# Performance work log

Measured on AMD Instinct MI355X. Metric: run time of the kernel, lower is better.

## Reference

```python
import jax, jax.numpy as jnp
import numpy as np
import math

B, S_IMG, S_TXT = 1, 2048, 256
D_MODEL, HEADS, HEAD_DIM = 3072, 24, 128
INNER = HEADS * HEAD_DIM
EPS = 1e-6


def _rmsnorm(x, scale):
    # flax-style RMSNorm over last dim, fp32 stats
    x32 = x.astype(jnp.float32)
    var = jnp.mean(x32 * x32, axis=-1, keepdims=True)
    return ((x32 * jax.lax.rsqrt(var + EPS)).astype(x.dtype)) * scale


def _rope(x, cos, sin):
    # x: [B,S,H,D]; cos,sin: [S,D]; interleaved-pair rotation (use_real_unbind_dim=-1)
    c = cos[None, :, None, :].astype(jnp.float32)
    s = sin[None, :, None, :].astype(jnp.float32)
    xp = x.reshape(*x.shape[:-1], -1, 2)
    x_rot = jnp.stack([-xp[..., 1], xp[..., 0]], axis=-1).reshape(x.shape)
    return (x.astype(jnp.float32) * c + x_rot.astype(jnp.float32) * s).astype(x.dtype)


def setup_inputs() -> dict:
    key = jax.random.key(0)
    ks = jax.random.split(key, 16)
    w = lambda k, shp: jax.random.normal(k, shp, jnp.float32) * 0.02
    S = S_TXT + S_IMG
    pos = jnp.arange(S, dtype=jnp.float32)
    inv_freq = 1.0 / (10000.0 ** (jnp.arange(0, HEAD_DIM, 2, dtype=jnp.float32) / HEAD_DIM))
    ang = pos[:, None] * inv_freq[None, :]  # [S, D/2]
    cos = jnp.repeat(jnp.cos(ang), 2, axis=-1)  # [S, D] paired layout
    sin = jnp.repeat(jnp.sin(ang), 2, axis=-1)
    return {
        'hidden_states': jax.random.normal(ks[0], (B, S_IMG, D_MODEL), jnp.float32),
        'encoder_hidden_states': jax.random.normal(ks[1], (B, S_TXT, D_MODEL), jnp.float32),
        'cos': cos,
        'sin': sin,
        'wq': w(ks[2], (D_MODEL, INNER)),
        'wk': w(ks[3], (D_MODEL, INNER)),
        'wv': w(ks[4], (D_MODEL, INNER)),
        'wq_add': w(ks[5], (D_MODEL, INNER)),
        'wk_add': w(ks[6], (D_MODEL, INNER)),
        'wv_add': w(ks[7], (D_MODEL, INNER)),
        'bq_add': w(ks[8], (INNER,)),
        'bk_add': w(ks[9], (INNER,)),
        'bv_add': w(ks[10], (INNER,)),
        'norm_q': jnp.ones((HEAD_DIM,), jnp.float32),
        'norm_k': jnp.ones((HEAD_DIM,), jnp.float32),
        'norm_add_q': jnp.ones((HEAD_DIM,), jnp.float32),
        'norm_add_k': jnp.ones((HEAD_DIM,), jnp.float32),
        'w_out': w(ks[11], (INNER, D_MODEL)),
        'b_out': w(ks[12], (D_MODEL,)),
        'w_add_out': w(ks[13], (INNER, D_MODEL)),
        'b_add_out': w(ks[14], (D_MODEL,)),
    }


def reference(hidden_states, encoder_hidden_states, cos, sin, wq, wk, wv,
              wq_add, wk_add, wv_add, bq_add, bk_add, bv_add,
              norm_q, norm_k, norm_add_q, norm_add_k,
              w_out, b_out, w_add_out, b_add_out):
    St = encoder_hidden_states.shape[1]
    heads = lambda x: x.reshape(x.shape[0], x.shape[1], HEADS, HEAD_DIM)
    # image-token q/k/v + QK RMSNorm
    q = _rmsnorm(heads(hidden_states @ wq), norm_q)
    k = _rmsnorm(heads(hidden_states @ wk), norm_k)
    v = heads(hidden_states @ wv)
    # encoder-token q/k/v (biased projections) + QK RMSNorm
    eq = _rmsnorm(heads(encoder_hidden_states @ wq_add + bq_add), norm_add_q)
    ek = _rmsnorm(heads(encoder_hidden_states @ wk_add + bk_add), norm_add_k)
    ev = heads(encoder_hidden_states @ wv_add + bv_add)
    # encoder tokens concatenated first
    q = jnp.concatenate([eq, q], axis=1)
    k = jnp.concatenate([ek, k], axis=1)
    v = jnp.concatenate([ev, v], axis=1)
    q = _rope(q, cos, sin)
    k = _rope(k, cos, sin)
    # naive softmax attention
    scale = 1.0 / math.sqrt(HEAD_DIM)
    attn = jnp.einsum('bshd,bthd->bhst', q, k) * scale
    attn = jax.nn.softmax(attn, axis=-1)
    out = jnp.einsum('bhst,bthd->bshd', attn, v)
    out = out.reshape(out.shape[0], out.shape[1], -1)
    # split back into encoder / image streams and apply output projections
    enc_out = out[:, :St] @ w_add_out + b_add_out
    img_out = out[:, St:] @ w_out + b_out
    return (img_out, enc_out)
```

## Files before the change

### kernel.cpp

```cpp
#include <hip/hip_runtime.h>
#include <hip/hip_bf16.h>

typedef unsigned short u16;
typedef unsigned int   u32;
typedef __bf16 bf16x8 __attribute__((ext_vector_type(8)));
typedef float  f32x4  __attribute__((ext_vector_type(4)));

#define SEQ   2304
#define DM    3072
#define NH    24
#define HD    128
#define S_TXT 256
#define S_IMG 2048
#define SCALE 0.08838834764831845f

__device__ __forceinline__ u16 f2bf(float x) {
  u32 u = __float_as_uint(x);
  u += 0x7fffu + ((u >> 16) & 1u);
  return (u16)(u >> 16);
}
__device__ __forceinline__ float bf2f(u16 b) {
  return __uint_as_float(((u32)b) << 16);
}
__device__ __forceinline__ f32x4 zero4() { f32x4 z = {0.f, 0.f, 0.f, 0.f}; return z; }
__device__ __forceinline__ u32 cvtpk(float lo, float hi) {
  u32 r;
  asm("v_cvt_pk_bf16_f32 %0, %1, %2" : "=v"(r) : "v"(lo), "v"(hi));
  return r;
}

#define GLDS16(gp, lp) __builtin_amdgcn_global_load_lds( \
    (__attribute__((address_space(1))) void*)(gp),       \
    (__attribute__((address_space(3))) void*)(lp), 16, 0, 0)

__global__ __launch_bounds__(256) void conv_bf16_k(const float* __restrict__ src,
                                                   u16* __restrict__ dst, int n4) {
  int i = blockIdx.x * 256 + threadIdx.x;
  if (i >= n4) return;
  float4 v = ((const float4*)src)[i];
  ushort4 o;
  o.x = f2bf(v.x); o.y = f2bf(v.y); o.z = f2bf(v.z); o.w = f2bf(v.w);
  ((ushort4*)dst)[i] = o;
}

struct WP { const float* s[8]; u16* d[8]; };

__global__ __launch_bounds__(256) void w_transpose_k(WP p) {
  __shared__ float tile[32][33];
  const float* __restrict__ src = p.s[blockIdx.z];
  u16* __restrict__ dst = p.d[blockIdx.z];
  const int c0 = blockIdx.x * 32, r0 = blockIdx.y * 32;
  const int tx = threadIdx.x & 31, ty = threadIdx.x >> 5;
#pragma unroll
  for (int i = 0; i < 4; ++i)
    tile[ty + i*8][tx] = src[(size_t)(r0 + ty + i*8) * DM + c0 + tx];
  __syncthreads();
#pragma unroll
  for (int i = 0; i < 4; ++i)
    dst[(size_t)(c0 + ty + i*8) * DM + r0 + tx] = f2bf(tile[tx][ty + i*8]);
}

__global__ __launch_bounds__(256) void v_transpose_k(const u16* __restrict__ V,
                                                     u16* __restrict__ Vt) {
  __shared__ u16 tile[32][34];
  const int h = blockIdx.z;
  const int t0 = blockIdx.x * 32, d0 = blockIdx.y * 32;
  const int tx = threadIdx.x & 31, ty = threadIdx.x >> 5;
#pragma unroll
  for (int i = 0; i < 4; ++i)
    tile[ty + i*8][tx] = V[((size_t)h * SEQ + t0 + ty + i*8) * HD + d0 + tx];
  __syncthreads();
#pragma unroll
  for (int i = 0; i < 4; ++i)
    Vt[((size_t)h * HD + d0 + ty + i*8) * SEQ + t0 + tx] = tile[tx][ty + i*8];
}

struct GArgs {
  const u16* A;
  const u16* Bimg0; const u16* Bimg1; const u16* Bimg2;
  const u16* Benc0; const u16* Benc1; const u16* Benc2;
  const float* bEnc0; const float* bEnc1; const float* bEnc2;
  const float* bImg;
  void* out0; void* out1; void* out2;
  int mode;
};

__global__ __launch_bounds__(256) void gemm_bt_k(GArgs p) {
  __shared__ __attribute__((aligned(128))) char As[128*128];
  __shared__ __attribute__((aligned(128))) char Bs[128*128];
  const int bz = blockIdx.z;
  const int bm = blockIdx.x, bn = blockIdx.y;
  const bool enc = (bm < 2);
  const u16* __restrict__ Bm = (bz == 0) ? (enc ? p.Benc0 : p.Bimg0)
                             : (bz == 1) ? (enc ? p.Benc1 : p.Bimg1)
                                         : (enc ? p.Benc2 : p.Bimg2);
  const float* __restrict__ bias = enc ? ((bz == 0) ? p.bEnc0 : (bz == 1) ? p.bEnc1 : p.bEnc2)
                                       : p.bImg;
  void* out = (bz == 0) ? p.out0 : (bz == 1) ? p.out1 : p.out2;
  const int tid = threadIdx.x;
  const int w = tid >> 6, l = tid & 63;
  const int wr = w >> 1, wc = w & 1;

  f32x4 acc[4][4];
#pragma unroll
  for (int mi = 0; mi < 4; ++mi)
#pragma unroll
    for (int ni = 0; ni < 4; ++ni) acc[mi][ni] = zero4();

  const int srow  = l >> 3;
  const int scolb = ((l & 7) ^ srow) << 4;
  const char* Ag = (const char*)(p.A + (size_t)(bm*128 + w*32) * DM) + (size_t)srow * (DM*2) + scolb;
  const char* Bg = (const char*)(Bm  + (size_t)(bn*128 + w*32) * DM) + (size_t)srow * (DM*2) + scolb;
  char* AsW = As + (w*32) * 128;
  char* BsW = Bs + (w*32) * 128;

  for (int kt = 0; kt < DM/64; ++kt) {
#pragma unroll
    for (int i = 0; i < 4; ++i) {
      GLDS16(Ag + (size_t)i*8*(DM*2) + kt*128, AsW + i*8*128);
      GLDS16(Bg + (size_t)i*8*(DM*2) + kt*128, BsW + i*8*128);
    }
    __syncthreads();
#pragma unroll
    for (int kk = 0; kk < 2; ++kk) {
      bf16x8 af[4], bfr[4];
#pragma unroll
      for (int mi = 0; mi < 4; ++mi) {
        const int row = wr*64 + mi*16 + (l & 15);
        const int cb  = ((kk << 6) + ((l >> 4) << 4)) ^ ((row & 7) << 4);
        af[mi] = *(const bf16x8*)(As + row*128 + cb);
      }
#pragma unroll
      for (int ni = 0; ni < 4; ++ni) {
        const int row = wc*64 + ni*16 + (l & 15);
        const int cb  = ((kk << 6) + ((l >> 4) << 4)) ^ ((row & 7) << 4);
        bfr[ni] = *(const bf16x8*)(Bs + row*128 + cb);
      }
#pragma unroll
      for (int mi = 0; mi < 4; ++mi)
#pragma unroll
        for (int ni = 0; ni < 4; ++ni)
          acc[mi][ni] = __builtin_amdgcn_mfma_f32_16x16x32_bf16(af[mi], bfr[ni], acc[mi][ni], 0, 0, 0);
    }
    __syncthreads();
  }

#pragma unroll
  for (int mi = 0; mi < 4; ++mi) {
    const int mbase = bm*128 + wr*64 + mi*16 + ((l >> 4) << 2);
#pragma unroll
    for (int ni = 0; ni < 4; ++ni) {
      const int ncol = bn*128 + wc*64 + ni*16 + (l & 15);
      const float bv = bias ? bias[ncol] : 0.f;
#pragma unroll
      for (int r = 0; r < 4; ++r) {
        const float v = acc[mi][ni][r] + bv;
        const int row = mbase + r;
        if (p.mode == 0) {
          ((u16*)out)[((size_t)bn * SEQ + row) * HD + (ncol & 127)] = f2bf(v);
        } else {
          const size_t orow = (row < S_TXT) ? (size_t)(S_IMG + row) : (size_t)(row - S_TXT);
          ((float*)out)[orow * DM + ncol] = v;
        }
      }
    }
  }
}

__global__ __launch_bounds__(256) void qk_norm_rope_k(
    const u16* __restrict__ Qf, const u16* __restrict__ Kf,
    u16* __restrict__ Qb, u16* __restrict__ Kb,
    const float* __restrict__ cosT, const float* __restrict__ sinT,
    const float* __restrict__ nq, const float* __restrict__ nk,
    const float* __restrict__ naq, const float* __restrict__ nak) {
  const int gw = (blockIdx.x * 256 + threadIdx.x) >> 6;
  const int l = threadIdx.x & 63;
  const int which = (gw >= NH * SEQ) ? 1 : 0;
  const int rem = which ? (gw - NH * SEQ) : gw;
  const int h = rem / SEQ, t = rem % SEQ;
  const size_t base = ((size_t)h * SEQ + t) * HD + l * 2;
  const ushort2 xb = *(const ushort2*)((which ? Kf : Qf) + base);
  const float x0 = bf2f(xb.x), x1 = bf2f(xb.y);
  float ss = x0*x0 + x1*x1;
#pragma unroll
  for (int msk = 1; msk < 64; msk <<= 1) ss += __shfl_xor(ss, msk, 64);
  const float rr = rsqrtf(ss * (1.0f/128.0f) + 1e-6f);
  const float* nw = which ? (t < S_TXT ? nak : nk) : (t < S_TXT ? naq : nq);
  const float n0 = x0 * rr * nw[l*2], n1 = x1 * rr * nw[l*2 + 1];
  const float c = cosT[(size_t)t * HD + l*2], sn = sinT[(size_t)t * HD + l*2];
  float o0 = n0 * c - n1 * sn;
  float o1 = n1 * c + n0 * sn;
  if (!which) { o0 *= SCALE; o1 *= SCALE; }
  ushort2 ob; ob.x = f2bf(o0); ob.y = f2bf(o1);
  *(ushort2*)((which ? Kb : Qb) + base) = ob;
}

__global__ __launch_bounds__(256) void attn_k(
    const u16* __restrict__ Q, const u16* __restrict__ K,
    const u16* __restrict__ Vt, u16* __restrict__ O) {
  __shared__ __attribute__((aligned(128))) char Kl[2][64*256];
  __shared__ __attribute__((aligned(128))) char Vl[2][128*128];
  __shared__ __attribute__((aligned(128))) char Pl[4][2048];
  const int orig = blockIdx.x;
  const int lin = (orig & 7) * 54 + (orig >> 3);
  const int h = lin / 18, qb = lin % 18;
  const int tid = threadIdx.x, w = tid >> 6, l = tid & 63;
  const int g = l >> 4, q16 = l & 15;
  const int NT = SEQ / 64;

  const u16* Qh = Q  + ((size_t)h * SEQ + qb*128 + w*32) * HD;
  const u16* Kh = K  + (size_t)h * SEQ * HD;
  const u16* Vh = Vt + (size_t)h * HD * SEQ;

  bf16x8 qf[2][4];
#pragma unroll
  for (int qt = 0; qt < 2; ++qt)
#pragma unroll
    for (int kf = 0; kf < 4; ++kf)
      qf[qt][kf] = *(const bf16x8*)(Qh + (qt*16 + q16) * HD + kf*32 + g*8);

  f32x4 o[2][8];
#pragma unroll
  for (int qt = 0; qt < 2; ++qt)
#pragma unroll
    for (int db = 0; db < 8; ++db) o[qt][db] = zero4();
  float m[2]  = {-3e38f, -3e38f};
  float rl[2] = {0.f, 0.f};

  const int vswz = ((l & 7) ^ (l >> 3)) << 4;
  const int pswz = (q16 & 7) << 4;

  auto STAGE = [&](int buf, int kb) {
#pragma unroll
    for (int i = 0; i < 4; ++i) {
      const int rloc = i*4 + (l >> 4);
      const int colb = ((l & 15) << 4) ^ ((rloc & 7) << 4);
      GLDS16((const char*)Kh + ((size_t)(kb*64 + w*16 + rloc)) * 256 + colb,
             &Kl[buf][(w*16 + i*4) * 256]);
    }
#pragma unroll
    for (int i = 0; i < 4; ++i) {
      const int rloc = w*32 + i*8 + (l >> 3);
      GLDS16((const char*)Vh + (size_t)rloc * (SEQ*2) + kb*128 + vswz,
             &Vl[buf][(w*32 + i*8) * 128]);
    }
  };

  STAGE(0, 0);
  int cur = 0;

  for (int kb = 0; kb < NT; ++kb) {
    if (kb + 1 < NT) {
      STAGE(cur ^ 1, kb + 1);
      asm volatile("s_waitcnt vmcnt(8)" ::: "memory");
    } else {
      asm volatile("s_waitcnt vmcnt(0)" ::: "memory");
    }
    __builtin_amdgcn_s_barrier();
    __builtin_amdgcn_sched_barrier(0);

    const char* Kb_ = Kl[cur];
    const char* Vb_ = Vl[cur];

    f32x4 s[2][4];
#pragma unroll
    for (int qt = 0; qt < 2; ++qt)
#pragma unroll
      for (int mi = 0; mi < 4; ++mi) s[qt][mi] = zero4();
    __builtin_amdgcn_s_setprio(1);
#pragma unroll
    for (int mi = 0; mi < 4; ++mi) {
      const int row = mi*16 + q16;
      bf16x8 kfr[4];
#pragma unroll
      for (int kf = 0; kf < 4; ++kf) {
        const int cb = ((kf << 6) + (g << 4)) ^ ((row & 7) << 4);
        kfr[kf] = *(const bf16x8*)(Kb_ + row*256 + cb);
      }
#pragma unroll
      for (int kf = 0; kf < 4; ++kf) {
        s[0][mi] = __builtin_amdgcn_mfma_f32_16x16x32_bf16(kfr[kf], qf[0][kf], s[0][mi], 0, 0, 0);
        s[1][mi] = __builtin_amdgcn_mfma_f32_16x16x32_bf16(kfr[kf], qf[1][kf], s[1][mi], 0, 0, 0);
      }
    }
    __builtin_amdgcn_s_setprio(0);

    float rsv[2];
    bf16x8 pa[2][2];
    char* Pw = Pl[w];
#pragma unroll
    for (int qt = 0; qt < 2; ++qt) {
      float mx = s[qt][0][0];
#pragma unroll
      for (int mi = 0; mi < 4; ++mi)
#pragma unroll
        for (int r = 0; r < 4; ++r) mx = fmaxf(mx, s[qt][mi][r]);
      mx = fmaxf(mx, __shfl_xor(mx, 16, 64));
      mx = fmaxf(mx, __shfl_xor(mx, 32, 64));
      const float mn = fmaxf(m[qt], mx);
      rsv[qt] = __expf(m[qt] - mn);
      m[qt] = mn;
      float sum = 0.f;
#pragma unroll
      for (int mi = 0; mi < 4; ++mi) {
        f32x4 t = s[qt][mi];
#pragma unroll
        for (int r = 0; r < 4; ++r) { t[r] = __expf(t[r] - mn); sum += t[r]; }
        s[qt][mi] = t;
      }
      sum += __shfl_xor(sum, 16, 64);
      sum += __shfl_xor(sum, 32, 64);
      rl[qt] = rl[qt] * rsv[qt] + sum;
#pragma unroll
      for (int mi = 0; mi < 4; ++mi) {
        uint2 pk;
        pk.x = cvtpk(s[qt][mi][0], s[qt][mi][1]);
        pk.y = cvtpk(s[qt][mi][2], s[qt][mi][3]);
        *(uint2*)(Pw + ((q16*128 + mi*32 + g*8) ^ pswz)) = pk;
      }
#pragma unroll
      for (int kblk = 0; kblk < 2; ++kblk)
        pa[qt][kblk] = *(const bf16x8*)(Pw + ((q16*128 + kblk*64 + g*16) ^ pswz));
    }

#pragma unroll
    for (int qt = 0; qt < 2; ++qt) {
      float rs4[4];
#pragma unroll
      for (int r = 0; r < 4; ++r)
        rs4[r] = __shfl(rsv[qt], (g << 4) + (g << 2) + r, 64);
#pragma unroll
      for (int db = 0; db < 8; ++db) {
        f32x4 t = o[qt][db];
#pragma unroll
        for (int r = 0; r < 4; ++r) t[r] *= rs4[r];
        o[qt][db] = t;
      }
    }

    __builtin_amdgcn_s_setprio(1);
#pragma unroll
    for (int kblk = 0; kblk < 2; ++kblk)
#pragma unroll
      for (int db = 0; db < 8; ++db) {
        const int vrow = db*16 + q16;
        const int vcb  = ((kblk << 6) + (g << 4)) ^ ((vrow & 7) << 4);
        bf16x8 vb = *(const bf16x8*)(Vb_ + vrow*128 + vcb);
        o[0][db] = __builtin_amdgcn_mfma_f32_16x16x32_bf16(pa[0][kblk], vb, o[0][db], 0, 0, 0);
        o[1][db] = __builtin_amdgcn_mfma_f32_16x16x32_bf16(pa[1][kblk], vb, o[1][db], 0, 0, 0);
      }
    __builtin_amdgcn_s_setprio(0);

    asm volatile("s_waitcnt lgkmcnt(0)" ::: "memory");
    __builtin_amdgcn_s_barrier();
    __builtin_amdgcn_sched_barrier(0);
    cur ^= 1;
  }

#pragma unroll
  for (int qt = 0; qt < 2; ++qt) {
    float inv4[4];
#pragma unroll
    for (int r = 0; r < 4; ++r)
      inv4[r] = 1.f / __shfl(rl[qt], (g << 4) + (g << 2) + r, 64);
#pragma unroll
    for (int db = 0; db < 8; ++db)
#pragma unroll
      for (int r = 0; r < 4; ++r) {
        const int token = qb*128 + w*32 + qt*16 + g*4 + r;
        const int col = h*HD + db*16 + q16;
        O[(size_t)token * DM + col] = f2bf(o[qt][db][r] * inv4[r]);
      }
  }
}

extern "C" void kernel_launch(void* const* d_in, const int* in_sizes, int n_in,
                              void* d_out, int out_size, void* d_ws, size_t ws_size,
                              hipStream_t stream) {
  const float* hidden = (const float*)d_in[0];
  const float* ench   = (const float*)d_in[1];
  const float* cosT   = (const float*)d_in[2];
  const float* sinT   = (const float*)d_in[3];
  const float* wq  = (const float*)d_in[4];
  const float* wk  = (const float*)d_in[5];
  const float* wv  = (const float*)d_in[6];
  const float* wqa = (const float*)d_in[7];
  const float* wka = (const float*)d_in[8];
  const float* wva = (const float*)d_in[9];
  const float* bqa = (const float*)d_in[10];
  const float* bka = (const float*)d_in[11];
  const float* bva = (const float*)d_in[12];
  const float* nq  = (const float*)d_in[13];
  const float* nk  = (const float*)d_in[14];
  const float* naq = (const float*)d_in[15];
  const float* nak = (const float*)d_in[16];
  const float* w_out     = (const float*)d_in[17];
  const float* b_out     = (const float*)d_in[18];
  const float* w_add_out = (const float*)d_in[19];
  const float* b_add_out = (const float*)d_in[20];
  float* outp = (float*)d_out;
  (void)in_sizes; (void)n_in; (void)out_size; (void)ws_size;

  char* ws = (char*)d_ws;
  size_t off = 0;
  auto alloc = [&](size_t n) { char* p = ws + off; off += (n + 255) & ~(size_t)255; return p; };
  u16* wt[8];
  for (int i = 0; i < 8; ++i) wt[i] = (u16*)alloc((size_t)DM * DM * 2);
  u16* xb = (u16*)alloc((size_t)SEQ * DM * 2);
  u16* Qf = (u16*)alloc((size_t)NH * SEQ * HD * 2);
  u16* Kf = (u16*)alloc((size_t)NH * SEQ * HD * 2);
  u16* Vf = (u16*)alloc((size_t)NH * SEQ * HD * 2);
  u16* Qb = (u16*)alloc((size_t)NH * SEQ * HD * 2);
  u16* Kb = (u16*)alloc((size_t)NH * SEQ * HD * 2);
  u16* Vt = (u16*)alloc((size_t)NH * HD * SEQ * 2);
  u16* Ob = (u16*)alloc((size_t)SEQ * DM * 2);

  conv_bf16_k<<<(S_TXT*DM/4)/256, 256, 0, stream>>>(ench, xb, S_TXT*DM/4);
  conv_bf16_k<<<(S_IMG*DM/4)/256, 256, 0, stream>>>(hidden, xb + (size_t)S_TXT*DM, S_IMG*DM/4);

  WP wp;
  wp.s[0] = wq;  wp.s[1] = wk;  wp.s[2] = wv;
  wp.s[3] = wqa; wp.s[4] = wka; wp.s[5] = wva;
  wp.s[6] = w_out; wp.s[7] = w_add_out;
  for (int i = 0; i < 8; ++i) wp.d[i] = wt[i];
  w_transpose_k<<<dim3(96, 96, 8), 256, 0, stream>>>(wp);

  GArgs qkv;
  qkv.A = xb;
  qkv.Bimg0 = wt[0]; qkv.Bimg1 = wt[1]; qkv.Bimg2 = wt[2];
  qkv.Benc0 = wt[3]; qkv.Benc1 = wt[4]; qkv.Benc2 = wt[5];
  qkv.bEnc0 = bqa;   qkv.bEnc1 = bka;   qkv.bEnc2 = bva;
  qkv.bImg  = nullptr;
  qkv.out0 = Qf; qkv.out1 = Kf; qkv.out2 = Vf;
  qkv.mode = 0;
  gemm_bt_k<<<dim3(18, 24, 3), 256, 0, stream>>>(qkv);

  qk_norm_rope_k<<<(2*NH*SEQ)/4, 256, 0, stream>>>(Qf, Kf, Qb, Kb, cosT, sinT, nq, nk, naq, nak);
  v_transpose_k<<<dim3(SEQ/32, HD/32, NH), 256, 0, stream>>>(Vf, Vt);

  attn_k<<<432, 256, 0, stream>>>(Qb, Kb, Vt, Ob);

  GArgs op;
  op.A = Ob;
  op.Bimg0 = wt[6]; op.Bimg1 = wt[6]; op.Bimg2 = wt[6];
  op.Benc0 = wt[7]; op.Benc1 = wt[7]; op.Benc2 = wt[7];
  op.bEnc0 = b_add_out; op.bEnc1 = b_add_out; op.bEnc2 = b_add_out;
  op.bImg  = b_out;
  op.out0 = outp; op.out1 = outp; op.out2 = outp;
  op.mode = 1;
  gemm_bt_k<<<dim3(18, 24, 1), 256, 0, stream>>>(op);
}
```

Before: 781.0 us.

## Fuse QK RMSNorm, RoPE and V transpose into QKV GEMM epilogue

Folds the per-head RMSNorm, rotary embedding and Q scaling into the QKV projection GEMM epilogue, reducing row sums across the two column waves through shared memory. The V output is written already transposed, which removes the separate norm/rope and V-transpose kernels and their intermediate buffers. It also swizzles the GEMM block order into 8 groups over a 1D grid and widens the weight transpose to 64x64 tiles with float4 loads. The epilogue gets heavier and writes Vt with strided ushort4 stores that may coalesce poorly.

```diff
diff --git a/kernel.cpp b/kernel.cpp
--- a/kernel.cpp
+++ b/kernel.cpp
@@ -46,33 +46,32 @@
 struct WP { const float* s[8]; u16* d[8]; };
 
 __global__ __launch_bounds__(256) void w_transpose_k(WP p) {
-  __shared__ float tile[32][33];
+  __shared__ float tile[64][65];
   const float* __restrict__ src = p.s[blockIdx.z];
   u16* __restrict__ dst = p.d[blockIdx.z];
-  const int c0 = blockIdx.x * 32, r0 = blockIdx.y * 32;
-  const int tx = threadIdx.x & 31, ty = threadIdx.x >> 5;
-#pragma unroll
-  for (int i = 0; i < 4; ++i)
-    tile[ty + i*8][tx] = src[(size_t)(r0 + ty + i*8) * DM + c0 + tx];
+  const int c0 = blockIdx.x * 64, r0 = blockIdx.y * 64;
+  const int tr = threadIdx.x >> 4;
+  const int tc = threadIdx.x & 15;
+#pragma unroll
+  for (int i = 0; i < 4; ++i) {
+    float4 v = *(const float4*)&src[(size_t)(r0 + i*16 + tr) * DM + c0 + tc*4];
+    tile[i*16 + tr][tc*4 + 0] = v.x;
+    tile[i*16 + tr][tc*4 + 1] = v.y;
+    tile[i*16 + tr][tc*4 + 2] = v.z;
+    tile[i*16 + tr][tc*4 + 3] = v.w;
+  }
   __syncthreads();
 #pragma unroll
-  for (int i = 0; i < 4; ++i)
-    dst[(size_t)(c0 + ty + i*8) * DM + r0 + tx] = f2bf(tile[tx][ty + i*8]);
-}
-
-__global__ __launch_bounds__(256) void v_transpose_k(const u16* __restrict__ V,
-                                                     u16* __restrict__ Vt) {
-  __shared__ u16 tile[32][34];
-  const int h = blockIdx.z;
-  const int t0 = blockIdx.x * 32, d0 = blockIdx.y * 32;
-  const int tx = threadIdx.x & 31, ty = threadIdx.x >> 5;
-#pragma unroll
-  for (int i = 0; i < 4; ++i)
-    tile[ty + i*8][tx] = V[((size_t)h * SEQ + t0 + ty + i*8) * HD + d0 + tx];
-  __syncthreads();
-#pragma unroll
-  for (int i = 0; i < 4; ++i)
-    Vt[((size_t)h * HD + d0 + ty + i*8) * SEQ + t0 + tx] = tile[tx][ty + i*8];
+  for (int j = 0; j < 4; ++j) {
+    const int nloc = j*16 + tr;
+    const int kloc = tc*4;
+    ushort4 o;
+    o.x = f2bf(tile[kloc + 0][nloc]);
+    o.y = f2bf(tile[kloc + 1][nloc]);
+    o.z = f2bf(tile[kloc + 2][nloc]);
+    o.w = f2bf(tile[kloc + 3][nloc]);
+    *(ushort4*)&dst[(size_t)(c0 + nloc) * DM + r0 + kloc] = o;
+  }
 }
 
 struct GArgs {
@@ -81,6 +80,8 @@
   const u16* Benc0; const u16* Benc1; const u16* Benc2;
   const float* bEnc0; const float* bEnc1; const float* bEnc2;
   const float* bImg;
+  const float* cosT; const float* sinT;
+  const float* nq; const float* nk; const float* naq; const float* nak;
   void* out0; void* out1; void* out2;
   int mode;
 };
@@ -88,8 +89,12 @@
 __global__ __launch_bounds__(256) void gemm_bt_k(GArgs p) {
   __shared__ __attribute__((aligned(128))) char As[128*128];
   __shared__ __attribute__((aligned(128))) char Bs[128*128];
-  const int bz = blockIdx.z;
-  const int bm = blockIdx.x, bn = blockIdx.y;
+  const int chunk = gridDim.x >> 3;
+  const int wg = (blockIdx.x & 7) * chunk + (blockIdx.x >> 3);
+  const int bm = wg % 18;
+  const int bt = wg / 18;
+  const int bn = bt % 24;
+  const int bz = bt / 24;
   const bool enc = (bm < 2);
   const u16* __restrict__ Bm = (bz == 0) ? (enc ? p.Benc0 : p.Bimg0)
                              : (bz == 1) ? (enc ? p.Benc1 : p.Bimg1)
@@ -100,6 +105,7 @@
   const int tid = threadIdx.x;
   const int w = tid >> 6, l = tid & 63;
   const int wr = w >> 1, wc = w & 1;
+  const int g = l >> 4, q16 = l & 15;
 
   f32x4 acc[4][4];
 #pragma unroll
@@ -126,14 +132,14 @@
       bf16x8 af[4], bfr[4];
 #pragma unroll
       for (int mi = 0; mi < 4; ++mi) {
-        const int row = wr*64 + mi*16 + (l & 15);
-        const int cb  = ((kk << 6) + ((l >> 4) << 4)) ^ ((row & 7) << 4);
+        const int row = wr*64 + mi*16 + q16;
+        const int cb  = ((kk << 6) + (g << 4)) ^ ((row & 7) << 4);
         af[mi] = *(const bf16x8*)(As + row*128 + cb);
       }
 #pragma unroll
       for (int ni = 0; ni < 4; ++ni) {
-        const int row = wc*64 + ni*16 + (l & 15);
-        const int cb  = ((kk << 6) + ((l >> 4) << 4)) ^ ((row & 7) << 4);
+        const int row = wc*64 + ni*16 + q16;
+        const int cb  = ((kk << 6) + (g << 4)) ^ ((row & 7) << 4);
         bfr[ni] = *(const bf16x8*)(Bs + row*128 + cb);
       }
 #pragma unroll
@@ -145,54 +151,95 @@
     __syncthreads();
   }
 
-#pragma unroll
-  for (int mi = 0; mi < 4; ++mi) {
-    const int mbase = bm*128 + wr*64 + mi*16 + ((l >> 4) << 2);
-#pragma unroll
-    for (int ni = 0; ni < 4; ++ni) {
-      const int ncol = bn*128 + wc*64 + ni*16 + (l & 15);
-      const float bv = bias ? bias[ncol] : 0.f;
-#pragma unroll
-      for (int r = 0; r < 4; ++r) {
-        const float v = acc[mi][ni][r] + bv;
-        const int row = mbase + r;
-        if (p.mode == 0) {
-          ((u16*)out)[((size_t)bn * SEQ + row) * HD + (ncol & 127)] = f2bf(v);
-        } else {
+  if (p.mode == 0) {
+    if (bias) {
+#pragma unroll
+      for (int ni = 0; ni < 4; ++ni) {
+        const float bv = bias[bn*128 + wc*64 + ni*16 + q16];
+#pragma unroll
+        for (int mi = 0; mi < 4; ++mi) {
+          f32x4 t = acc[mi][ni];
+#pragma unroll
+          for (int r = 0; r < 4; ++r) t[r] += bv;
+          acc[mi][ni] = t;
+        }
+      }
+    }
+    if (bz == 2) {
+      u16* Vt_ = (u16*)out;
+#pragma unroll
+      for (int mi = 0; mi < 4; ++mi) {
+        const int tb = bm*128 + wr*64 + mi*16 + g*4;
+#pragma unroll
+        for (int ni = 0; ni < 4; ++ni) {
+          const int col = wc*64 + ni*16 + q16;
+          ushort4 o4;
+          o4.x = f2bf(acc[mi][ni][0]); o4.y = f2bf(acc[mi][ni][1]);
+          o4.z = f2bf(acc[mi][ni][2]); o4.w = f2bf(acc[mi][ni][3]);
+          *(ushort4*)&Vt_[((size_t)bn*HD + col)*SEQ + tb] = o4;
+        }
+      }
+    } else {
+      float ss[4][4];
+#pragma unroll
+      for (int mi = 0; mi < 4; ++mi)
+#pragma unroll
+        for (int r = 0; r < 4; ++r) {
+          float v = 0.f;
+#pragma unroll
+          for (int ni = 0; ni < 4; ++ni) v += acc[mi][ni][r] * acc[mi][ni][r];
+#pragma unroll
+          for (int msk = 1; msk < 16; msk <<= 1) v += __shfl_xor(v, msk, 64);
+          ss[mi][r] = v;
+        }
+      float* red = (float*)As;
+      if (q16 == 0) {
+#pragma unroll
+        for (int mi = 0; mi < 4; ++mi)
+#pragma unroll
+          for (int r = 0; r < 4; ++r)
+            red[w*64 + mi*16 + g*4 + r] = ss[mi][r];
+      }
+      __syncthreads();
+      const float* nw = (bz == 0) ? (enc ? p.naq : p.nq) : (enc ? p.nak : p.nk);
+      u16* O_ = (u16*)out;
+#pragma unroll
+      for (int mi = 0; mi < 4; ++mi)
+#pragma unroll
+        for (int r = 0; r < 4; ++r) {
+          const float tot = ss[mi][r] + red[(w^1)*64 + mi*16 + g*4 + r];
+          const float rr = rsqrtf(tot * (1.0f/128.0f) + 1e-6f);
+          const int t = bm*128 + wr*64 + mi*16 + g*4 + r;
+#pragma unroll
+          for (int ni = 0; ni < 4; ++ni) {
+            const int col = wc*64 + ni*16 + q16;
+            const float xn = acc[mi][ni][r] * rr * nw[col];
+            const float pt = __shfl_xor(xn, 1, 64);
+            const float c  = p.cosT[(size_t)t*HD + col];
+            const float sn = p.sinT[(size_t)t*HD + col];
+            float o = (q16 & 1) ? (xn*c + pt*sn) : (xn*c - pt*sn);
+            if (bz == 0) o *= SCALE;
+            O_[((size_t)bn*SEQ + t)*HD + col] = f2bf(o);
+          }
+        }
+    }
+  } else {
+#pragma unroll
+    for (int mi = 0; mi < 4; ++mi) {
+      const int mbase = bm*128 + wr*64 + mi*16 + g*4;
+#pragma unroll
+      for (int ni = 0; ni < 4; ++ni) {
+        const int ncol = bn*128 + wc*64 + ni*16 + q16;
+        const float bv = bias ? bias[ncol] : 0.f;
+#pragma unroll
+        for (int r = 0; r < 4; ++r) {
+          const int row = mbase + r;
           const size_t orow = (row < S_TXT) ? (size_t)(S_IMG + row) : (size_t)(row - S_TXT);
-          ((float*)out)[orow * DM + ncol] = v;
+          ((float*)out)[orow * DM + ncol] = acc[mi][ni][r] + bv;
         }
       }
     }
   }
-}
-
-__global__ __launch_bounds__(256) void qk_norm_rope_k(
-    const u16* __restrict__ Qf, const u16* __restrict__ Kf,
-    u16* __restrict__ Qb, u16* __restrict__ Kb,
-    const float* __restrict__ cosT, const float* __restrict__ sinT,
-    const float* __restrict__ nq, const float* __restrict__ nk,
-    const float* __restrict__ naq, const float* __restrict__ nak) {
-  const int gw = (blockIdx.x * 256 + threadIdx.x) >> 6;
-  const int l = threadIdx.x & 63;
-  const int which = (gw >= NH * SEQ) ? 1 : 0;
-  const int rem = which ? (gw - NH * SEQ) : gw;
-  const int h = rem / SEQ, t = rem % SEQ;
-  const size_t base = ((size_t)h * SEQ + t) * HD + l * 2;
-  const ushort2 xb = *(const ushort2*)((which ? Kf : Qf) + base);
-  const float x0 = bf2f(xb.x), x1 = bf2f(xb.y);
-  float ss = x0*x0 + x1*x1;
-#pragma unroll
-  for (int msk = 1; msk < 64; msk <<= 1) ss += __shfl_xor(ss, msk, 64);
-  const float rr = rsqrtf(ss * (1.0f/128.0f) + 1e-6f);
-  const float* nw = which ? (t < S_TXT ? nak : nk) : (t < S_TXT ? naq : nq);
-  const float n0 = x0 * rr * nw[l*2], n1 = x1 * rr * nw[l*2 + 1];
-  const float c = cosT[(size_t)t * HD + l*2], sn = sinT[(size_t)t * HD + l*2];
-  float o0 = n0 * c - n1 * sn;
-  float o1 = n1 * c + n0 * sn;
-  if (!which) { o0 *= SCALE; o1 *= SCALE; }
-  ushort2 ob; ob.x = f2bf(o0); ob.y = f2bf(o1);
-  *(ushort2*)((which ? Kb : Qb) + base) = ob;
 }
 
 __global__ __launch_bounds__(256) void attn_k(
@@ -407,9 +454,6 @@
   u16* wt[8];
   for (int i = 0; i < 8; ++i) wt[i] = (u16*)alloc((size_t)DM * DM * 2);
   u16* xb = (u16*)alloc((size_t)SEQ * DM * 2);
-  u16* Qf = (u16*)alloc((size_t)NH * SEQ * HD * 2);
-  u16* Kf = (u16*)alloc((size_t)NH * SEQ * HD * 2);
-  u16* Vf = (u16*)alloc((size_t)NH * SEQ * HD * 2);
   u16* Qb = (u16*)alloc((size_t)NH * SEQ * HD * 2);
   u16* Kb = (u16*)alloc((size_t)NH * SEQ * HD * 2);
   u16* Vt = (u16*)alloc((size_t)NH * HD * SEQ * 2);
@@ -423,7 +467,7 @@
   wp.s[3] = wqa; wp.s[4] = wka; wp.s[5] = wva;
   wp.s[6] = w_out; wp.s[7] = w_add_out;
   for (int i = 0; i < 8; ++i) wp.d[i] = wt[i];
-  w_transpose_k<<<dim3(96, 96, 8), 256, 0, stream>>>(wp);
+  w_transpose_k<<<dim3(48, 48, 8), 256, 0, stream>>>(wp);
 
   GArgs qkv;
   qkv.A = xb;
@@ -431,12 +475,11 @@
   qkv.Benc0 = wt[3]; qkv.Benc1 = wt[4]; qkv.Benc2 = wt[5];
   qkv.bEnc0 = bqa;   qkv.bEnc1 = bka;   qkv.bEnc2 = bva;
   qkv.bImg  = nullptr;
-  qkv.out0 = Qf; qkv.out1 = Kf; qkv.out2 = Vf;
+  qkv.cosT = cosT; qkv.sinT = sinT;
+  qkv.nq = nq; qkv.nk = nk; qkv.naq = naq; qkv.nak = nak;
+  qkv.out0 = Qb; qkv.out1 = Kb; qkv.out2 = Vt;
   qkv.mode = 0;
-  gemm_bt_k<<<dim3(18, 24, 3), 256, 0, stream>>>(qkv);
-
-  qk_norm_rope_k<<<(2*NH*SEQ)/4, 256, 0, stream>>>(Qf, Kf, Qb, Kb, cosT, sinT, nq, nk, naq, nak);
-  v_transpose_k<<<dim3(SEQ/32, HD/32, NH), 256, 0, stream>>>(Vf, Vt);
+  gemm_bt_k<<<1296, 256, 0, stream>>>(qkv);
 
   attn_k<<<432, 256, 0, stream>>>(Qb, Kb, Vt, Ob);
 
@@ -446,7 +489,9 @@
   op.Benc0 = wt[7]; op.Benc1 = wt[7]; op.Benc2 = wt[7];
   op.bEnc0 = b_add_out; op.bEnc1 = b_add_out; op.bEnc2 = b_add_out;
   op.bImg  = b_out;
+  op.cosT = nullptr; op.sinT = nullptr;
+  op.nq = nullptr; op.nk = nullptr; op.naq = nullptr; op.nak = nullptr;
   op.out0 = outp; op.out1 = outp; op.out2 = outp;
   op.mode = 1;
-  gemm_bt_k<<<dim3(18, 24, 1), 256, 0, stream>>>(op);
-}
+  gemm_bt_k<<<432, 256, 0, stream>>>(op);
+}
```

After: 808.4 us. +3.5%, slower.
